# Performance work log

Hardware: AMD Instinct MI355X
Metric: run time of the kernel (lower is better)

The kernel has to match this reference:

```python
import jax, jax.numpy as jnp
import numpy as np

B, C, H, W = 8, 512, 32, 32
N = H * W
FG_THRES, BG_THRES, TOPK = 0.7, 0.6, 12


def setup_inputs() -> dict:
    key = jax.random.key(0)
    k1, k2, k3 = jax.random.split(key, 3)
    feature_q = jax.random.normal(k1, (B, C, H, W), dtype=jnp.float32)
    support_feat = jax.random.normal(k2, (B, C, H, W), dtype=jnp.float32)
    support_mask = jax.random.randint(k3, (B, H, W), 0, 2).astype(jnp.int32)
    return {"feature_q": feature_q, "support_feat": support_feat, "support_mask": support_mask}


def _masked_avg_pool(feat, mask):
    # feat [B,C,H,W], mask [B,1,H,W]; interpolate to same size is identity
    return jnp.sum(feat * mask, axis=(2, 3)) / (jnp.sum(mask, axis=(2, 3)) + 1e-5)


def _cosine(a, b):
    # F.cosine_similarity along channel dim 1 (eps=1e-8), with broadcasting
    dot = jnp.sum(a * b, axis=1)
    na = jnp.sqrt(jnp.sum(a * a, axis=1))
    nb = jnp.sqrt(jnp.sum(b * b, axis=1))
    return dot / jnp.maximum(na * nb, 1e-8)


def _similarity(feature_q, fg_proto, bg_proto):
    sim_fg = _cosine(feature_q, fg_proto)
    sim_bg = _cosine(feature_q, bg_proto)
    return jnp.stack([sim_bg, sim_fg], axis=1) * 10.0  # [B,2,H,W]


def _select_weights(pred, thres):
    # pred [N] -> float {0,1} selection weights; threshold mask, topk-12 fallback
    m = pred > thres
    _, top_idx = jax.lax.top_k(pred, TOPK)
    tm = jnp.zeros_like(m).at[top_idx].set(True)
    return jnp.where(m.sum() > 0, m, tm).astype(pred.dtype)


def _ssp_single(cur_feat, pred_fg, pred_bg):
    # cur_feat [C,N]; masked formulation == torch's variable-length column select
    wf = _select_weights(pred_fg, FG_THRES)
    wb = _select_weights(pred_bg, BG_THRES)
    fg_proto = jnp.sum(cur_feat * wf, axis=-1) / wf.sum()  # [C]
    bg_proto = jnp.sum(cur_feat * wb, axis=-1) / wb.sum()
    cn = cur_feat / jnp.sqrt(jnp.sum(cur_feat * cur_feat, axis=0, keepdims=True))
    sim = (cn.T @ cn) * 2.0  # [N,N] cosine sim, scaled
    neg = jnp.asarray(-1e30, sim.dtype)
    fg_attn = jax.nn.softmax(jnp.where(wf[None, :] > 0, sim, neg), axis=-1)
    bg_attn = jax.nn.softmax(jnp.where(wb[None, :] > 0, sim, neg), axis=-1)
    fg_local = (fg_attn @ cur_feat.T).T  # [C,N]
    bg_local = (bg_attn @ cur_feat.T).T
    return fg_proto, bg_proto, fg_local, bg_local


def reference(feature_q, support_feat, support_mask):
    mask_f = (support_mask == 1).astype(feature_q.dtype)[:, None]  # [B,1,H,W]
    mask_b = (support_mask == 0).astype(feature_q.dtype)[:, None]
    FP = _masked_avg_pool(support_feat, mask_f)[:, :, None, None]  # [B,C,1,1]
    BP = _masked_avg_pool(support_feat, mask_b)[:, :, None, None]
    out_0 = _similarity(feature_q, FP, BP)  # [B,2,H,W]
    pred = jax.nn.softmax(out_0, axis=1).reshape(B, 2, N)
    cur = feature_q.reshape(B, C, N)
    fg_p, bg_p, fg_l, bg_l = jax.vmap(_ssp_single)(cur, pred[:, 1], pred[:, 0])
    SSFP = fg_p[:, :, None, None]
    SSBP = bg_p[:, :, None, None]
    ASBP = bg_l.reshape(B, C, H, W)
    FP_1 = FP * 0.5 + SSFP * 0.5
    BP_1 = SSBP * 0.3 + ASBP * 0.7
    out_1 = _similarity(feature_q, FP_1, BP_1)  # [B,2,H,W]
    return out_1
```

## Files before the change

kernel.cpp:

```cpp
#include <hip/hip_runtime.h>
#include <math.h>

#define Bsz 8
#define Cch 512
#define Npx 1024
#define TOPK 12
#define BN (Bsz * Npx)

typedef __attribute__((ext_vector_type(8))) short bf16x8;
typedef __attribute__((ext_vector_type(4))) float f32x4;

__device__ __forceinline__ unsigned short f2bf(float x) {
    unsigned u = __float_as_uint(x);
    u += 0x7FFF + ((u >> 16) & 1);
    return (unsigned short)(u >> 16);
}
__device__ __forceinline__ float bf2f(unsigned short h) {
    return __uint_as_float(((unsigned)h) << 16);
}

__device__ __forceinline__ float warp_sum64(float v) {
    for (int o = 32; o > 0; o >>= 1) v += __shfl_down(v, o);
    return v;
}
__device__ __forceinline__ float block_sum512(float v, float* s8) {
    v = warp_sum64(v);
    int lane = threadIdx.x & 63, w = threadIdx.x >> 6;
    __syncthreads();
    if (lane == 0) s8[w] = v;
    __syncthreads();
    float r = 0.f;
    #pragma unroll
    for (int k = 0; k < 8; k++) r += s8[k];
    return r;
}

__global__ void k_pool(const float* __restrict__ sf, const int* __restrict__ mask,
                       float* __restrict__ FPo, float* __restrict__ BPo) {
    __shared__ float s4a[4], s4b[4], s4c[4];
    int c = blockIdx.x, b = blockIdx.y, t = threadIdx.x;
    const float4* f4 = (const float4*)(sf + ((size_t)b * Cch + c) * Npx);
    const int4* m4 = (const int4*)(mask + (size_t)b * Npx);
    float4 v = f4[t];
    int4 m = m4[t];
    float sumf = (m.x == 1 ? v.x : 0.f) + (m.y == 1 ? v.y : 0.f)
               + (m.z == 1 ? v.z : 0.f) + (m.w == 1 ? v.w : 0.f);
    float tot = v.x + v.y + v.z + v.w;
    float cf = (float)((m.x == 1) + (m.y == 1) + (m.z == 1) + (m.w == 1));
    sumf = warp_sum64(sumf);
    tot  = warp_sum64(tot);
    cf   = warp_sum64(cf);
    int lane = t & 63, w = t >> 6;
    if (lane == 0) { s4a[w] = sumf; s4b[w] = tot; s4c[w] = cf; }
    __syncthreads();
    if (t == 0) {
        float sA = s4a[0] + s4a[1] + s4a[2] + s4a[3];
        float sB = s4b[0] + s4b[1] + s4b[2] + s4b[3];
        float sC = s4c[0] + s4c[1] + s4c[2] + s4c[3];
        FPo[b * Cch + c] = sA / (sC + 1e-5f);
        BPo[b * Cch + c] = (sB - sA) / ((1024.f - sC) + 1e-5f);
    }
}

__global__ void __launch_bounds__(512) k_predcast(const float* __restrict__ fq,
                       const float* __restrict__ FP, const float* __restrict__ BP,
                       float* __restrict__ dsim, float* __restrict__ invn,
                       unsigned short* __restrict__ Ft) {
    __shared__ float sFP[Cch], sBP[Cch], s8[8];
    __shared__ float rdf[16][32], rdb[16][32], rqq[16][32];
    __shared__ unsigned short S[32][522];
    int b = blockIdx.y, t = threadIdx.x;
    int tx = t & 31, ty = t >> 5;
    int p0 = blockIdx.x * 32;
    int p = p0 + tx;
    sFP[t] = FP[b * Cch + t];
    sBP[t] = BP[b * Cch + t];
    __syncthreads();
    float nf = sqrtf(block_sum512(sFP[t] * sFP[t], s8));
    float nb = sqrtf(block_sum512(sBP[t] * sBP[t], s8));
    const float* q = fq + (size_t)b * Cch * Npx + p;
    float df = 0.f, db = 0.f, qq = 0.f;
    int c0 = ty * 32;
    #pragma unroll 4
    for (int c = 0; c < 32; c += 2) {
        float v0 = q[(size_t)(c0 + c) * Npx];
        float v1 = q[(size_t)(c0 + c + 1) * Npx];
        df += v0 * sFP[c0 + c] + v1 * sFP[c0 + c + 1];
        db += v0 * sBP[c0 + c] + v1 * sBP[c0 + c + 1];
        qq += v0 * v0 + v1 * v1;
        unsigned pk = (unsigned)f2bf(v0) | ((unsigned)f2bf(v1) << 16);
        *(unsigned*)&S[tx][c0 + c] = pk;
    }
    rdf[ty][tx] = df; rdb[ty][tx] = db; rqq[ty][tx] = qq;
    __syncthreads();
    for (int s = 8; s > 0; s >>= 1) {
        if (ty < s) {
            rdf[ty][tx] += rdf[ty + s][tx];
            rdb[ty][tx] += rdb[ty + s][tx];
            rqq[ty][tx] += rqq[ty + s][tx];
        }
        __syncthreads();
    }
    if (ty == 0) {
        float nq = sqrtf(rqq[0][tx]);
        float simf = 10.f * rdf[0][tx] / fmaxf(nq * nf, 1e-8f);
        float simb = 10.f * rdb[0][tx] / fmaxf(nq * nb, 1e-8f);
        dsim[b * Npx + p] = simf - simb;
        invn[b * Npx + p] = 1.f / nq;
    }
    int w = t >> 6, lane = t & 63;
    unsigned short* FtB = Ft + (size_t)b * Npx * Cch;
    for (int pr = w; pr < 32; pr += 8) {
        unsigned* dst = (unsigned*)(FtB + (size_t)(p0 + pr) * Cch);
        #pragma unroll
        for (int it = 0; it < 4; it++) {
            int d = it * 64 + lane;
            dst[d] = *(const unsigned*)&S[pr][d * 2];
        }
    }
}

__global__ void __launch_bounds__(1024) k_selcompact(const float* __restrict__ dsim,
                        const float* __restrict__ invn,
                        const unsigned short* __restrict__ Ft,
                        const float* __restrict__ FP,
                        int* __restrict__ nsf, int* __restrict__ nsb,
                        int* __restrict__ jf, int* __restrict__ jb,
                        float* __restrict__ ivg,
                        float* __restrict__ fgp, float* __restrict__ bgp,
                        float* __restrict__ FP1, float* __restrict__ nfv) {
    __shared__ int wsum[16];
    __shared__ int sns;
    __shared__ float sProto[16][512];
    __shared__ float s16f[16];
    int b = blockIdx.y, t = threadIdx.x;
    int lane = t & 63, w = t >> 6;
    bool isf = (blockIdx.x == 0);
    float d = dsim[b * Npx + t];
    float key = isf ? d : -d;
    float thres = isf ? 0.8472979f : 0.4054651f;
    int flag = (key > thres) ? 1 : 0;
    int x = flag;
    #pragma unroll
    for (int o = 1; o < 64; o <<= 1) {
        int y = __shfl_up(x, o);
        if (lane >= o) x += y;
    }
    if (lane == 63) wsum[w] = x;
    __syncthreads();
    int base = 0, total = 0;
    #pragma unroll
    for (int k = 0; k < 16; k++) {
        int s = wsum[k];
        if (k < w) base += s;
        total += s;
    }
    int* jdst = (isf ? jf : jb) + b * Npx;
    if (total == 0) {
        __shared__ int   sc[Npx];
        __shared__ float v[Npx];
        __shared__ float rv[Npx];
        __shared__ int   ri[Npx];
        v[t] = key; flag = 0;
        __syncthreads();
        for (int k = 0; k < TOPK; k++) {
            rv[t] = v[t]; ri[t] = t;
            __syncthreads();
            for (int s = 512; s > 0; s >>= 1) {
                if (t < s) {
                    float a = rv[t], bb = rv[t + s];
                    int ia = ri[t], ib = ri[t + s];
                    if (bb > a || (bb == a && ib < ia)) { rv[t] = bb; ri[t] = ib; }
                }
                __syncthreads();
            }
            int win = ri[0];
            if (t == win) { flag = 1; v[t] = -INFINITY; }
            __syncthreads();
        }
        sc[t] = flag;
        __syncthreads();
        for (int off = 1; off < 1024; off <<= 1) {
            int xx = (t >= off) ? sc[t - off] : 0;
            __syncthreads();
            sc[t] += xx;
            __syncthreads();
        }
        if (flag) {
            int pos = sc[t] - 1;
            jdst[pos] = t;
            if (!isf) ivg[b * Npx + pos] = invn[b * Npx + t];
        }
        if (t == 1023) sns = sc[1023];
    } else {
        if (flag) {
            int pos = base + x - 1;
            jdst[pos] = t;
            if (!isf) ivg[b * Npx + pos] = invn[b * Npx + t];
        }
        if (t == 0) sns = total;
    }
    __syncthreads();
    int ns = sns;
    if (t == 0) (isf ? nsf : nsb)[b] = ns;
    const unsigned short* FtB = Ft + (size_t)b * Npx * Cch;
    float facc[8] = {0.f, 0.f, 0.f, 0.f, 0.f, 0.f, 0.f, 0.f};
    int k = w;
    int row = (k < ns) ? jdst[k] : 0;
    while (k < ns) {
        int kn = k + 16;
        int rown = (kn < ns) ? jdst[kn] : 0;
        bf16x8 vv = *(const bf16x8*)&FtB[(size_t)row * Cch + lane * 8];
        #pragma unroll
        for (int e = 0; e < 8; e++) facc[e] += bf2f((unsigned short)vv[e]);
        k = kn; row = rown;
    }
    #pragma unroll
    for (int e = 0; e < 8; e++) sProto[w][lane * 8 + e] = facc[e];
    __syncthreads();
    float fp1 = 0.f;
    if (t < 512) {
        float s = 0.f;
        #pragma unroll
        for (int q = 0; q < 16; q++) s += sProto[q][t];
        float pv = s / (float)ns;
        (isf ? fgp : bgp)[b * Cch + t] = pv;
        if (isf) {
            fp1 = 0.5f * FP[b * Cch + t] + 0.5f * pv;
            FP1[b * Cch + t] = fp1;
        }
    }
    if (isf) {
        float v2 = warp_sum64(fp1 * fp1);
        if (lane == 0) s16f[w] = v2;
        __syncthreads();
        if (t == 0) {
            float nn = 0.f;
            #pragma unroll
            for (int q = 0; q < 16; q++) nn += s16f[q];
            nfv[b] = sqrtf(nn);
        }
    }
}

__global__ void __launch_bounds__(512) k_fused(
        const unsigned short* __restrict__ Ft,
        const int* __restrict__ jb, const int* __restrict__ nsb,
        const float* __restrict__ invn, const float* __restrict__ ivg,
        const float* __restrict__ bgp, const float* __restrict__ FP1,
        const float* __restrict__ nfv, float* __restrict__ out) {
    __shared__ unsigned short Afull[32][520];
    __shared__ unsigned short sP[32][1032];
    __shared__ unsigned short Bt2[2][64][136];
    __shared__ int   sji[1024];
    __shared__ float sfj[1024];
    __shared__ float sfp1full[Cch], sbgfull[Cch];
    __shared__ float sfi[32], sden[32];
    __shared__ float spart[32][4];

    int bid = blockIdx.x;
    int b = bid & 7;
    int i0 = (bid >> 3) * 32;
    int tid = threadIdx.x;
    int l = tid & 63, w = tid >> 6;
    int ml = l & 15, quad = l >> 4;
    int ns = nsb[b];
    int K64 = ((((ns + 31) & ~31) + 63) & ~63);
    int T = K64 >> 6;

    const unsigned short* FtB = Ft + (size_t)b * Npx * Cch;

    #pragma unroll
    for (int s = 0; s < 4; s++) {
        int idx = tid + s * 512;
        int row = idx >> 6, kc8 = (idx & 63) * 8;
        *(uint4*)&Afull[row][kc8] = *(const uint4*)(FtB + (size_t)(i0 + row) * Cch + kc8);
    }
    for (int j = tid; j < K64; j += 512) {
        sji[j] = (j < ns) ? jb[b * Npx + j] : jb[b * Npx];
        sfj[j] = (j < ns) ? ivg[b * Npx + j] : 0.f;
    }
    sfp1full[tid] = FP1[b * Cch + tid];
    sbgfull[tid]  = 0.3f * bgp[b * Cch + tid];
    if (tid < 32) sfi[tid] = 2.f * invn[b * Npx + i0 + tid];
    __syncthreads();

    int ig = w & 1, jg = w >> 1;
    int grow = tid >> 4, gk8 = (tid & 15) * 8;
    for (int j0 = 0; j0 < K64; j0 += 64) {
        const unsigned short* pb0 = FtB + (size_t)sji[j0 + grow] * Cch + gk8;
        const unsigned short* pb1 = FtB + (size_t)sji[j0 + 32 + grow] * Cch + gk8;
        uint4 v0 = *(const uint4*)pb0;
        uint4 v1 = *(const uint4*)pb1;
        f32x4 acc = {};
        #pragma unroll
        for (int kt = 0; kt < 4; kt++) {
            int buf = kt & 1;
            *(uint4*)&Bt2[buf][grow][gk8] = v0;
            *(uint4*)&Bt2[buf][32 + grow][gk8] = v1;
            int kn = (kt + 1) * 128;
            if (kn < Cch) {
                v0 = *(const uint4*)(pb0 + kn);
                v1 = *(const uint4*)(pb1 + kn);
            }
            __syncthreads();
            int k0 = kt * 128;
            #pragma unroll
            for (int h = 0; h < 4; h++) {
                bf16x8 af = *(const bf16x8*)&Afull[ig * 16 + ml][k0 + h * 32 + quad * 8];
                bf16x8 bf = *(const bf16x8*)&Bt2[buf][jg * 16 + ml][h * 32 + quad * 8];
                acc = __builtin_amdgcn_mfma_f32_16x16x32_bf16(af, bf, acc, 0, 0, 0);
            }
        }
        #pragma unroll
        for (int r = 0; r < 4; r++) {
            int il = ig * 16 + quad * 4 + r;
            int jl = jg * 16 + ml;
            float e = (j0 + jl < ns) ? __expf(acc[r] * sfi[il] * sfj[j0 + jl]) : 0.f;
            sP[il][j0 + jl] = f2bf(e);
        }
    }
    __syncthreads();

    {
        int i = tid >> 4, jj16 = tid & 15;
        float s = 0.f;
        for (int j = jj16; j < K64; j += 16) s += bf2f(sP[i][j]);
        #pragma unroll
        for (int m = 1; m < 16; m <<= 1) s += __shfl_xor(s, m);
        if (jj16 == 0) sden[i] = s;
    }
    if (tid < 128) ((float*)spart)[tid] = 0.f;
    __syncthreads();

    int cgw = w & 3, igw = w >> 2;
    int icol = igw * 16 + ml;
    float rdi = 1.f / sden[icol];
    float sdb = 0.f, snb = 0.f, sdf = 0.f, sqq = 0.f;
    int jj = tid & 63, cg = tid >> 6;
    for (int c0 = 0; c0 < Cch; c0 += 64) {
        f32x4 accp = {};
        uint4 vv = *(const uint4*)(FtB + (size_t)sji[jj] * Cch + c0 + cg * 8);
        for (int jt = 0; jt < T; jt++) {
            int buf = jt & 1;
            {
                unsigned short* qd = &Bt2[buf][cg * 8][jj];
                qd[0]       = (unsigned short)vv.x;  qd[136]     = (unsigned short)(vv.x >> 16);
                qd[2 * 136] = (unsigned short)vv.y;  qd[3 * 136] = (unsigned short)(vv.y >> 16);
                qd[4 * 136] = (unsigned short)vv.z;  qd[5 * 136] = (unsigned short)(vv.z >> 16);
                qd[6 * 136] = (unsigned short)vv.w;  qd[7 * 136] = (unsigned short)(vv.w >> 16);
            }
            if (jt + 1 < T)
                vv = *(const uint4*)(FtB + (size_t)sji[(jt + 1) * 64 + jj] * Cch + c0 + cg * 8);
            __syncthreads();
            int j0 = jt * 64;
            #pragma unroll
            for (int hh = 0; hh < 2; hh++) {
                bf16x8 af  = *(const bf16x8*)&Bt2[buf][cgw * 16 + ml][hh * 32 + quad * 8];
                bf16x8 bfr = *(const bf16x8*)&sP[icol][j0 + hh * 32 + quad * 8];
                accp = __builtin_amdgcn_mfma_f32_16x16x32_bf16(af, bfr, accp, 0, 0, 0);
            }
        }
        #pragma unroll
        for (int r = 0; r < 4; r++) {
            int cl = c0 + cgw * 16 + quad * 4 + r;
            float loc = accp[r] * rdi;
            float bp1 = sbgfull[cl] + 0.7f * loc;
            float qv = bf2f(Afull[icol][cl]);
            sdb += qv * bp1;
            snb += bp1 * bp1;
            sdf += qv * sfp1full[cl];
            sqq += qv * qv;
        }
        __syncthreads();
    }
    sdb += __shfl_xor(sdb, 16);  sdb += __shfl_xor(sdb, 32);
    snb += __shfl_xor(snb, 16);  snb += __shfl_xor(snb, 32);
    sdf += __shfl_xor(sdf, 16);  sdf += __shfl_xor(sdf, 32);
    sqq += __shfl_xor(sqq, 16);  sqq += __shfl_xor(sqq, 32);
    if (quad == 0) {
        atomicAdd(&spart[icol][0], sdb);
        atomicAdd(&spart[icol][1], snb);
        atomicAdd(&spart[icol][2], sdf);
        atomicAdd(&spart[icol][3], sqq);
    }
    __syncthreads();
    if (tid < 32) {
        float db = spart[tid][0], nb = spart[tid][1];
        float df = spart[tid][2], qq = spart[tid][3];
        float nq = sqrtf(qq);
        float sb2 = 10.f * db / fmaxf(nq * sqrtf(nb), 1e-8f);
        float sf2 = 10.f * df / fmaxf(nq * nfv[b], 1e-8f);
        out[((size_t)b * 2) * Npx + i0 + tid] = sb2;
        out[((size_t)b * 2 + 1) * Npx + i0 + tid] = sf2;
    }
}

extern "C" void kernel_launch(void* const* d_in, const int* in_sizes, int n_in,
                              void* d_out, int out_size, void* d_ws, size_t ws_size,
                              hipStream_t stream) {
    const float* fq = (const float*)d_in[0];
    const float* sf = (const float*)d_in[1];
    const int* mask = (const int*)d_in[2];
    float* out = (float*)d_out;

    float* ws = (float*)d_ws;
    float* FP    = ws;
    float* BP    = FP + Bsz * Cch;
    float* fgp   = BP + Bsz * Cch;
    float* bgp   = fgp + Bsz * Cch;
    float* FP1   = bgp + Bsz * Cch;
    float* nfv   = FP1 + Bsz * Cch;
    float* dsim  = nfv + 8;
    float* invn  = dsim + BN;
    float* ivg   = invn + BN;
    int*   nsf   = (int*)(ivg + BN);
    int*   nsb   = nsf + 8;
    int*   jf    = nsb + 8;
    int*   jb    = jf + BN;
    unsigned short* Ft = (unsigned short*)(jb + BN);

    k_pool<<<dim3(Cch, Bsz), 256, 0, stream>>>(sf, mask, FP, BP);
    k_predcast<<<dim3(Npx / 32, Bsz), 512, 0, stream>>>(fq, FP, BP, dsim, invn, Ft);
    k_selcompact<<<dim3(2, Bsz), 1024, 0, stream>>>(dsim, invn, Ft, FP, nsf, nsb, jf, jb, ivg, fgp, bgp, FP1, nfv);
    k_fused<<<dim3(256), 512, 0, stream>>>(Ft, jb, nsb, invn, ivg, bgp, FP1, nfv, out);
}
```

Measured before the change: 126.5 us.

## Restructure attention-value GEMM to stage full-channel V tiles and reuse P fragments

Replaces the per-64-channel outer loop (which re-streamed all selected rows T times per channel chunk) with a single pass over key tiles, where each thread loads two full 32-channel row segments and writes a transposed 512x64 V tile into a shared buffer aliased with the old A/B tile storage. Each wave now keeps 4x2 MFMA accumulators covering 64 channels by 32 queries, so each V fragment is reused across both query halves and barrier count drops from T per chunk to two per tile. The query norm is taken from the precomputed inverse norm instead of a separate sum of squares, and query values are read from global memory in the epilogue. This raises register pressure and uses more shared memory per tile.

New measurement: 125.1 us. Within noise of the previous version (-1.1%).

```diff
diff --git a/kernel.cpp b/kernel.cpp
--- a/kernel.cpp
+++ b/kernel.cpp
@@ -249,14 +249,17 @@
         const float* __restrict__ invn, const float* __restrict__ ivg,
         const float* __restrict__ bgp, const float* __restrict__ FP1,
         const float* __restrict__ nfv, float* __restrict__ out) {
-    __shared__ unsigned short Afull[32][520];
+    __shared__ unsigned short U[36864];
     __shared__ unsigned short sP[32][1032];
-    __shared__ unsigned short Bt2[2][64][136];
     __shared__ int   sji[1024];
     __shared__ float sfj[1024];
     __shared__ float sfp1full[Cch], sbgfull[Cch];
     __shared__ float sfi[32], sden[32];
-    __shared__ float spart[32][4];
+    __shared__ float spart[32][3];
+
+    unsigned short (*Afull)[520] = (unsigned short(*)[520])U;
+    unsigned short (*Bt2)[64][136] = (unsigned short(*)[64][136])(U + 16640);
+    unsigned short (*Vt)[72] = (unsigned short(*)[72])U;
 
     int bid = blockIdx.x;
     int b = bid & 7;
@@ -330,65 +333,97 @@
         for (int m = 1; m < 16; m <<= 1) s += __shfl_xor(s, m);
         if (jj16 == 0) sden[i] = s;
     }
-    if (tid < 128) ((float*)spart)[tid] = 0.f;
-    __syncthreads();
-
-    int cgw = w & 3, igw = w >> 2;
-    int icol = igw * 16 + ml;
-    float rdi = 1.f / sden[icol];
-    float sdb = 0.f, snb = 0.f, sdf = 0.f, sqq = 0.f;
-    int jj = tid & 63, cg = tid >> 6;
-    for (int c0 = 0; c0 < Cch; c0 += 64) {
-        f32x4 accp = {};
-        uint4 vv = *(const uint4*)(FtB + (size_t)sji[jj] * Cch + c0 + cg * 8);
-        for (int jt = 0; jt < T; jt++) {
-            int buf = jt & 1;
-            {
-                unsigned short* qd = &Bt2[buf][cg * 8][jj];
-                qd[0]       = (unsigned short)vv.x;  qd[136]     = (unsigned short)(vv.x >> 16);
-                qd[2 * 136] = (unsigned short)vv.y;  qd[3 * 136] = (unsigned short)(vv.y >> 16);
-                qd[4 * 136] = (unsigned short)vv.z;  qd[5 * 136] = (unsigned short)(vv.z >> 16);
-                qd[6 * 136] = (unsigned short)vv.w;  qd[7 * 136] = (unsigned short)(vv.w >> 16);
-            }
-            if (jt + 1 < T)
-                vv = *(const uint4*)(FtB + (size_t)sji[(jt + 1) * 64 + jj] * Cch + c0 + cg * 8);
-            __syncthreads();
-            int j0 = jt * 64;
+    if (tid < 96) ((float*)spart)[tid] = 0.f;
+    __syncthreads();
+
+    int jp = tid & 31, cgg = tid >> 5;
+    f32x4 accp[4][2] = {};
+    const unsigned short* rA = FtB + (size_t)sji[2 * jp] * Cch + cgg * 32;
+    const unsigned short* rB = FtB + (size_t)sji[2 * jp + 1] * Cch + cgg * 32;
+    uint4 a0 = *(const uint4*)rA, a1 = *(const uint4*)(rA + 8);
+    uint4 a2 = *(const uint4*)(rA + 16), a3 = *(const uint4*)(rA + 24);
+    uint4 b0 = *(const uint4*)rB, b1 = *(const uint4*)(rB + 8);
+    uint4 b2 = *(const uint4*)(rB + 16), b3 = *(const uint4*)(rB + 24);
+    for (int jt = 0; jt < T; jt++) {
+        {
+            unsigned ad[16] = {a0.x, a0.y, a0.z, a0.w, a1.x, a1.y, a1.z, a1.w,
+                               a2.x, a2.y, a2.z, a2.w, a3.x, a3.y, a3.z, a3.w};
+            unsigned bd[16] = {b0.x, b0.y, b0.z, b0.w, b1.x, b1.y, b1.z, b1.w,
+                               b2.x, b2.y, b2.z, b2.w, b3.x, b3.y, b3.z, b3.w};
             #pragma unroll
-            for (int hh = 0; hh < 2; hh++) {
-                bf16x8 af  = *(const bf16x8*)&Bt2[buf][cgw * 16 + ml][hh * 32 + quad * 8];
-                bf16x8 bfr = *(const bf16x8*)&sP[icol][j0 + hh * 32 + quad * 8];
-                accp = __builtin_amdgcn_mfma_f32_16x16x32_bf16(af, bfr, accp, 0, 0, 0);
-            }
-        }
-        #pragma unroll
-        for (int r = 0; r < 4; r++) {
-            int cl = c0 + cgw * 16 + quad * 4 + r;
-            float loc = accp[r] * rdi;
-            float bp1 = sbgfull[cl] + 0.7f * loc;
-            float qv = bf2f(Afull[icol][cl]);
-            sdb += qv * bp1;
-            snb += bp1 * bp1;
-            sdf += qv * sfp1full[cl];
-            sqq += qv * qv;
-        }
-        __syncthreads();
-    }
-    sdb += __shfl_xor(sdb, 16);  sdb += __shfl_xor(sdb, 32);
-    snb += __shfl_xor(snb, 16);  snb += __shfl_xor(snb, 32);
-    sdf += __shfl_xor(sdf, 16);  sdf += __shfl_xor(sdf, 32);
-    sqq += __shfl_xor(sqq, 16);  sqq += __shfl_xor(sqq, 32);
-    if (quad == 0) {
-        atomicAdd(&spart[icol][0], sdb);
-        atomicAdd(&spart[icol][1], snb);
-        atomicAdd(&spart[icol][2], sdf);
-        atomicAdd(&spart[icol][3], sqq);
+            for (int d = 0; d < 16; d++) {
+                int c = cgg * 32 + 2 * d;
+                *(unsigned*)&Vt[c][2 * jp]     = (ad[d] & 0xFFFFu) | (bd[d] << 16);
+                *(unsigned*)&Vt[c + 1][2 * jp] = (ad[d] >> 16) | (bd[d] & 0xFFFF0000u);
+            }
+        }
+        if (jt + 1 < T) {
+            rA = FtB + (size_t)sji[(jt + 1) * 64 + 2 * jp] * Cch + cgg * 32;
+            rB = FtB + (size_t)sji[(jt + 1) * 64 + 2 * jp + 1] * Cch + cgg * 32;
+            a0 = *(const uint4*)rA; a1 = *(const uint4*)(rA + 8);
+            a2 = *(const uint4*)(rA + 16); a3 = *(const uint4*)(rA + 24);
+            b0 = *(const uint4*)rB; b1 = *(const uint4*)(rB + 8);
+            b2 = *(const uint4*)(rB + 16); b3 = *(const uint4*)(rB + 24);
+        }
+        __syncthreads();
+        int j0 = jt * 64;
+        #pragma unroll
+        for (int iff = 0; iff < 2; iff++) {
+            bf16x8 p0 = *(const bf16x8*)&sP[iff * 16 + ml][j0 + quad * 8];
+            bf16x8 p1 = *(const bf16x8*)&sP[iff * 16 + ml][j0 + 32 + quad * 8];
+            #pragma unroll
+            for (int cf = 0; cf < 4; cf++) {
+                bf16x8 v0 = *(const bf16x8*)&Vt[w * 64 + cf * 16 + ml][quad * 8];
+                bf16x8 v1 = *(const bf16x8*)&Vt[w * 64 + cf * 16 + ml][32 + quad * 8];
+                accp[cf][iff] = __builtin_amdgcn_mfma_f32_16x16x32_bf16(v0, p0, accp[cf][iff], 0, 0, 0);
+                accp[cf][iff] = __builtin_amdgcn_mfma_f32_16x16x32_bf16(v1, p1, accp[cf][iff], 0, 0, 0);
+            }
+        }
+        __syncthreads();
+    }
+
+    float sdb[2] = {0.f, 0.f}, snb[2] = {0.f, 0.f}, sdf[2] = {0.f, 0.f};
+    #pragma unroll
+    for (int iff = 0; iff < 2; iff++) {
+        int icol = iff * 16 + ml;
+        float rdi = 1.f / sden[icol];
+        #pragma unroll
+        for (int cf = 0; cf < 4; cf++) {
+            int clb = w * 64 + cf * 16 + quad * 4;
+            const unsigned* qp = (const unsigned*)(FtB + (size_t)(i0 + icol) * Cch + clb);
+            unsigned q01 = qp[0], q23 = qp[1];
+            float qv[4] = { bf2f((unsigned short)(q01 & 0xFFFFu)),
+                            bf2f((unsigned short)(q01 >> 16)),
+                            bf2f((unsigned short)(q23 & 0xFFFFu)),
+                            bf2f((unsigned short)(q23 >> 16)) };
+            #pragma unroll
+            for (int r = 0; r < 4; r++) {
+                int cl = clb + r;
+                float loc = accp[cf][iff][r] * rdi;
+                float bp1 = sbgfull[cl] + 0.7f * loc;
+                sdb[iff] += qv[r] * bp1;
+                snb[iff] += bp1 * bp1;
+                sdf[iff] += qv[r] * sfp1full[cl];
+            }
+        }
+    }
+    #pragma unroll
+    for (int iff = 0; iff < 2; iff++) {
+        float a = sdb[iff], bq = snb[iff], c = sdf[iff];
+        a += __shfl_xor(a, 16);  a += __shfl_xor(a, 32);
+        bq += __shfl_xor(bq, 16); bq += __shfl_xor(bq, 32);
+        c += __shfl_xor(c, 16);  c += __shfl_xor(c, 32);
+        if (quad == 0) {
+            int icol = iff * 16 + ml;
+            atomicAdd(&spart[icol][0], a);
+            atomicAdd(&spart[icol][1], bq);
+            atomicAdd(&spart[icol][2], c);
+        }
     }
     __syncthreads();
     if (tid < 32) {
-        float db = spart[tid][0], nb = spart[tid][1];
-        float df = spart[tid][2], qq = spart[tid][3];
-        float nq = sqrtf(qq);
+        float db = spart[tid][0], nb = spart[tid][1], df = spart[tid][2];
+        float nq = 2.f / sfi[tid];
         float sb2 = 10.f * db / fmaxf(nq * sqrtf(nb), 1e-8f);
         float sf2 = 10.f * df / fmaxf(nq * nfv[b], 1e-8f);
         out[((size_t)b * 2) * Npx + i0 + tid] = sb2;
```
